# Optimization experiments

Measured on AMD Instinct MI355X. Metric: run time of the kernel, lower is better.

The kernel has to match this reference:

```python
import jax, jax.numpy as jnp
import numpy as np
from jax import lax

SIGMA, RHO, BETA = 10.0, 28.0, 8.0 / 3.0
DT = 0.01
LEN_VAR = 3
BATCH = 262144
T_STEPS = 64


def lorenz(x, t):
    # x: [3, B] -> dx/dt: [3, B]  (autonomous; t unused, kept for signature fidelity)
    xx, yy, zz = x[0], x[1], x[2]
    return jnp.stack([SIGMA * (yy - xx),
                      xx * (RHO - zz) - yy,
                      xx * yy - BETA * zz])


def tangent_propagator(x, dt):
    # Jfunc: returns I + dt * J(x), shape [3, 3, B]
    xx, yy, zz = x[0], x[1], x[2]
    o = jnp.ones_like(xx)
    z = jnp.zeros_like(xx)
    J = jnp.stack([
        jnp.stack([-SIGMA * o, SIGMA * o, z]),
        jnp.stack([RHO - zz, -o, -xx]),
        jnp.stack([yy, xx, -BETA * o]),
    ])  # [3,3,B]
    eye = jnp.eye(LEN_VAR, dtype=x.dtype)[:, :, None]
    return eye + dt * J


def ode4(x, t, dt):
    k1 = lorenz(x, t)
    k2 = lorenz(x + dt * 0.5 * k1, t + dt * 0.5)
    k3 = lorenz(x + dt * 0.5 * k2, t + dt * 0.5)
    # NOTE: faithful to original bug — k4 evaluated at x + dt*k2 (not k3)
    k4 = lorenz(x + dt * k2, t + dt)
    return x + dt * (k1 + 2.0 * k2 + 2.0 * k3 + k4) * (1.0 / 6.0)


def mgs_rows(M):
    # Modified Gram-Schmidt over rows of M: [lv, lv, B].
    # Matches in-place torch semantics: row kase is projected against the
    # already-orthogonalized (unnormalized) earlier rows.
    rows = [M[i] for i in range(LEN_VAR)]
    for kase in range(LEN_VAR):
        a = rows[kase]
        for i in range(kase):
            b = rows[i]
            coef = jnp.sum(b * a, axis=0) / jnp.sum(b * b, axis=0)  # [B]
            a = a - coef * b
        rows[kase] = a
    return jnp.stack(rows)  # [lv, lv, B]


def setup_inputs() -> dict:
    key = jax.random.key(0)
    x = jax.random.normal(key, (LEN_VAR, BATCH), dtype=jnp.float32)
    time_sequ = (jnp.arange(T_STEPS, dtype=jnp.float32) * DT)
    return {"x": x, "time_sequ": time_sequ}


def reference(x, time_sequ):
    dt = jnp.asarray(DT, dtype=x.dtype)
    B = x.shape[1]
    Q0 = jnp.broadcast_to(jnp.eye(LEN_VAR, dtype=x.dtype)[:, :, None],
                          (LEN_VAR, LEN_VAR, B))
    lya0 = jnp.zeros((LEN_VAR, B), dtype=x.dtype)

    def step(carry, t):
        xs, Q, lya = carry
        xs = ode4(xs, t, dt)
        J = tangent_propagator(xs, dt)           # [3,3,B]
        Q = jnp.einsum('ikb,kjb->ijb', J, Q)      # Jaco @ eye, per trajectory
        Q = mgs_rows(Q)
        norm = jnp.sqrt(jnp.sum(Q * Q, axis=1))   # [3,B] row norms
        Q = Q / norm[:, None, :]
        lya = (lya * t + jnp.log(norm)) / (t + dt)
        return (xs, Q, lya), None

    (xf, Qf, lya), _ = lax.scan(step, (x, Q0, lya0), time_sequ)
    return lya, xf
```

## Files before the change

kernel.cpp:

```cpp
#include <hip/hip_runtime.h>

#define SIGMA 10.0f
#define RHO   28.0f
#define DT    0.01f
static constexpr float BETA = (float)(8.0 / 3.0);
#define HALF_LN2 0.34657359028f

typedef float v2 __attribute__((ext_vector_type(2)));

__device__ __forceinline__ v2 vsplat(float s) { v2 r; r.x = s; r.y = s; return r; }
__device__ __forceinline__ v2 vfma(v2 a, v2 b, v2 c) {
    return __builtin_elementwise_fma(a, b, c);
}
__device__ __forceinline__ v2 sfma(float s, v2 a, v2 c) {
    return __builtin_elementwise_fma(vsplat(s), a, c);
}
__device__ __forceinline__ v2 vdot3(v2 a0, v2 a1, v2 a2, v2 b0, v2 b1, v2 b2) {
    return vfma(a2, b2, vfma(a1, b1, a0 * b0));
}
__device__ __forceinline__ v2 vrsq(v2 a) {
    v2 r;
    r.x = __builtin_amdgcn_rsqf(a.x);
    r.y = __builtin_amdgcn_rsqf(a.y);
    return r;
}

__device__ __forceinline__ void lorenz_v(v2 x, v2 y, v2 z,
                                         v2& dx, v2& dy, v2& dz) {
    dx = vsplat(SIGMA) * (y - x);
    dy = x * (vsplat(RHO) - z) - y;
    dz = x * y - vsplat(BETA) * z;
}

__global__ __launch_bounds__(256, 2)
void lya_spec_kernel(const float* __restrict__ xin,
                     const float* __restrict__ ts,
                     float* __restrict__ out,
                     int B, int T) {
    const int i = blockIdx.x * blockDim.x + threadIdx.x;
    if (2 * i >= B) return;

    v2 x = ((const v2*)(xin))[i];
    v2 y = ((const v2*)(xin + B))[i];
    v2 z = ((const v2*)(xin + 2 * B))[i];

    v2 q00 = vsplat(1.f), q01 = vsplat(0.f), q02 = vsplat(0.f);
    v2 q10 = vsplat(0.f), q11 = vsplat(1.f), q12 = vsplat(0.f);
    v2 q20 = vsplat(0.f), q21 = vsplat(0.f), q22 = vsplat(1.f);

    v2 pr0 = vsplat(1.f), pr1 = vsplat(1.f), pr2 = vsplat(1.f);

    for (int it = 0; it < T; ++it) {
        v2 k1x, k1y, k1z, k2x, k2y, k2z, k3x, k3y, k3z, k4x, k4y, k4z;
        lorenz_v(x, y, z, k1x, k1y, k1z);
        const float h = DT * 0.5f;
        lorenz_v(sfma(h, k1x, x), sfma(h, k1y, y), sfma(h, k1z, z), k2x, k2y, k2z);
        lorenz_v(sfma(h, k2x, x), sfma(h, k2y, y), sfma(h, k2z, z), k3x, k3y, k3z);
        lorenz_v(sfma(DT, k2x, x), sfma(DT, k2y, y), sfma(DT, k2z, z), k4x, k4y, k4z);
        const float c6 = DT * (float)(1.0 / 6.0);
        x = sfma(c6, (k1x + k4x) + vsplat(2.f) * (k2x + k3x), x);
        y = sfma(c6, (k1y + k4y) + vsplat(2.f) * (k2y + k3y), y);
        z = sfma(c6, (k1z + k4z) + vsplat(2.f) * (k2z + k3z), z);

        const float j00 = 1.0f - DT * SIGMA;
        const float j01 = DT * SIGMA;
        const float j11 = 1.0f - DT;
        const float j22 = 1.0f - DT * BETA;
        v2 j10 = vsplat(DT) * (vsplat(RHO) - z);
        v2 j12 = vsplat(-DT) * x;
        v2 j20 = vsplat(DT) * y;
        v2 j21 = vsplat(DT) * x;

        v2 n00 = sfma(j01, q10, vsplat(j00) * q00);
        v2 n01 = sfma(j01, q11, vsplat(j00) * q01);
        v2 n02 = sfma(j01, q12, vsplat(j00) * q02);
        v2 n10 = vfma(j12, q20, sfma(j11, q10, j10 * q00));
        v2 n11 = vfma(j12, q21, sfma(j11, q11, j10 * q01));
        v2 n12 = vfma(j12, q22, sfma(j11, q12, j10 * q02));
        v2 n20 = sfma(j22, q20, vfma(j21, q10, j20 * q00));
        v2 n21 = sfma(j22, q21, vfma(j21, q11, j20 * q01));
        v2 n22 = sfma(j22, q22, vfma(j21, q12, j20 * q02));

        v2 d00 = vdot3(n00, n01, n02, n00, n01, n02);
        v2 rn0 = vrsq(d00);
        v2 rd00 = rn0 * rn0;

        v2 d01 = vdot3(n00, n01, n02, n10, n11, n12);
        v2 c01 = d01 * rd00;
        v2 r10 = n10 - c01 * n00;
        v2 r11 = n11 - c01 * n01;
        v2 r12 = n12 - c01 * n02;

        v2 d02 = vdot3(n00, n01, n02, n20, n21, n22);
        v2 c02 = d02 * rd00;
        v2 a0 = n20 - c02 * n00;
        v2 a1 = n21 - c02 * n01;
        v2 a2 = n22 - c02 * n02;

        v2 d11 = vdot3(r10, r11, r12, r10, r11, r12);
        v2 rn1 = vrsq(d11);
        v2 d1a = vdot3(r10, r11, r12, a0, a1, a2);
        v2 c12 = d1a * (rn1 * rn1);
        v2 r20 = a0 - c12 * r10;
        v2 r21 = a1 - c12 * r11;
        v2 r22 = a2 - c12 * r12;

        v2 d22 = vdot3(r20, r21, r22, r20, r21, r22);
        v2 rn2 = vrsq(d22);

        pr0 = pr0 * d00;
        pr1 = pr1 * d11;
        pr2 = pr2 * d22;

        q00 = n00 * rn0; q01 = n01 * rn0; q02 = n02 * rn0;
        q10 = r10 * rn1; q11 = r11 * rn1; q12 = r12 * rn1;
        q20 = r20 * rn2; q21 = r21 * rn2; q22 = r22 * rn2;
    }

    const float denom = ts[T - 1] + DT;
    const float rden = __builtin_amdgcn_rcpf(denom) * HALF_LN2;
    v2 l0, l1, l2;
    l0.x = __builtin_amdgcn_logf(pr0.x) * rden;
    l0.y = __builtin_amdgcn_logf(pr0.y) * rden;
    l1.x = __builtin_amdgcn_logf(pr1.x) * rden;
    l1.y = __builtin_amdgcn_logf(pr1.y) * rden;
    l2.x = __builtin_amdgcn_logf(pr2.x) * rden;
    l2.y = __builtin_amdgcn_logf(pr2.y) * rden;

    ((v2*)(out))[i]          = l0;
    ((v2*)(out + B))[i]      = l1;
    ((v2*)(out + 2 * B))[i]  = l2;
    ((v2*)(out + 3 * B))[i]  = x;
    ((v2*)(out + 4 * B))[i]  = y;
    ((v2*)(out + 5 * B))[i]  = z;
}

extern "C" void kernel_launch(void* const* d_in, const int* in_sizes, int n_in,
                              void* d_out, int out_size, void* d_ws, size_t ws_size,
                              hipStream_t stream) {
    const float* xin = (const float*)d_in[0];
    const float* ts  = (const float*)d_in[1];
    float* out = (float*)d_out;

    const int B = in_sizes[0] / 3;
    const int T = in_sizes[1];

    const int block = 256;
    const int pairs = B / 2;
    const int grid = (pairs + block - 1) / block;
    lya_spec_kernel<<<grid, block, 0, stream>>>(xin, ts, out, B, T);
}
```

Baseline: 87.87 us.

## Software-pipeline RK4 one step ahead and compute Gram-Schmidt via Gram matrix

The RK4 state update for the next step is hoisted so it runs interleaved with the tangent-space QR of the current step, giving the scheduler two independent dependency chains to overlap. Modified Gram-Schmidt is recomputed from the 3x3 Gram matrix of the propagated rows, so all dot products are independent and the rsq chain is shorter. The cost is one extra RK4 evaluation per thread and altered floating-point rounding from the Gram-matrix formulation, which can lose accuracy when rows become nearly dependent.

```diff
diff --git a/kernel.cpp b/kernel.cpp
--- a/kernel.cpp
+++ b/kernel.cpp
@@ -32,6 +32,19 @@
     dz = x * y - vsplat(BETA) * z;
 }
 
+__device__ __forceinline__ void rk4(v2& x, v2& y, v2& z) {
+    v2 k1x, k1y, k1z, k2x, k2y, k2z, k3x, k3y, k3z, k4x, k4y, k4z;
+    lorenz_v(x, y, z, k1x, k1y, k1z);
+    const float h = DT * 0.5f;
+    lorenz_v(sfma(h, k1x, x), sfma(h, k1y, y), sfma(h, k1z, z), k2x, k2y, k2z);
+    lorenz_v(sfma(h, k2x, x), sfma(h, k2y, y), sfma(h, k2z, z), k3x, k3y, k3z);
+    lorenz_v(sfma(DT, k2x, x), sfma(DT, k2y, y), sfma(DT, k2z, z), k4x, k4y, k4z);
+    const float c6 = DT * (float)(1.0 / 6.0);
+    x = sfma(c6, (k1x + k4x) + vsplat(2.f) * (k2x + k3x), x);
+    y = sfma(c6, (k1y + k4y) + vsplat(2.f) * (k2y + k3y), y);
+    z = sfma(c6, (k1z + k4z) + vsplat(2.f) * (k2z + k3z), z);
+}
+
 __global__ __launch_bounds__(256, 2)
 void lya_spec_kernel(const float* __restrict__ xin,
                      const float* __restrict__ ts,
@@ -40,9 +53,9 @@
     const int i = blockIdx.x * blockDim.x + threadIdx.x;
     if (2 * i >= B) return;
 
-    v2 x = ((const v2*)(xin))[i];
-    v2 y = ((const v2*)(xin + B))[i];
-    v2 z = ((const v2*)(xin + 2 * B))[i];
+    v2 xn = ((const v2*)(xin))[i];
+    v2 yn = ((const v2*)(xin + B))[i];
+    v2 zn = ((const v2*)(xin + 2 * B))[i];
 
     v2 q00 = vsplat(1.f), q01 = vsplat(0.f), q02 = vsplat(0.f);
     v2 q10 = vsplat(0.f), q11 = vsplat(1.f), q12 = vsplat(0.f);
@@ -50,26 +63,18 @@
 
     v2 pr0 = vsplat(1.f), pr1 = vsplat(1.f), pr2 = vsplat(1.f);
 
+    rk4(xn, yn, zn);
+    v2 xo = xn, yo = yn, zo = zn;
+
     for (int it = 0; it < T; ++it) {
-        v2 k1x, k1y, k1z, k2x, k2y, k2z, k3x, k3y, k3z, k4x, k4y, k4z;
-        lorenz_v(x, y, z, k1x, k1y, k1z);
-        const float h = DT * 0.5f;
-        lorenz_v(sfma(h, k1x, x), sfma(h, k1y, y), sfma(h, k1z, z), k2x, k2y, k2z);
-        lorenz_v(sfma(h, k2x, x), sfma(h, k2y, y), sfma(h, k2z, z), k3x, k3y, k3z);
-        lorenz_v(sfma(DT, k2x, x), sfma(DT, k2y, y), sfma(DT, k2z, z), k4x, k4y, k4z);
-        const float c6 = DT * (float)(1.0 / 6.0);
-        x = sfma(c6, (k1x + k4x) + vsplat(2.f) * (k2x + k3x), x);
-        y = sfma(c6, (k1y + k4y) + vsplat(2.f) * (k2y + k3y), y);
-        z = sfma(c6, (k1z + k4z) + vsplat(2.f) * (k2z + k3z), z);
-
         const float j00 = 1.0f - DT * SIGMA;
         const float j01 = DT * SIGMA;
         const float j11 = 1.0f - DT;
         const float j22 = 1.0f - DT * BETA;
-        v2 j10 = vsplat(DT) * (vsplat(RHO) - z);
-        v2 j12 = vsplat(-DT) * x;
-        v2 j20 = vsplat(DT) * y;
-        v2 j21 = vsplat(DT) * x;
+        v2 j10 = vsplat(DT) * (vsplat(RHO) - zn);
+        v2 j12 = vsplat(-DT) * xn;
+        v2 j20 = vsplat(DT) * yn;
+        v2 j21 = vsplat(DT) * xn;
 
         v2 n00 = sfma(j01, q10, vsplat(j00) * q00);
         v2 n01 = sfma(j01, q11, vsplat(j00) * q01);
@@ -81,36 +86,38 @@
         v2 n21 = sfma(j22, q21, vfma(j21, q11, j20 * q01));
         v2 n22 = sfma(j22, q22, vfma(j21, q12, j20 * q02));
 
-        v2 d00 = vdot3(n00, n01, n02, n00, n01, n02);
-        v2 rn0 = vrsq(d00);
+        xo = xn; yo = yn; zo = zn;
+        rk4(xn, yn, zn);
+
+        v2 g00 = vdot3(n00, n01, n02, n00, n01, n02);
+        v2 g01 = vdot3(n00, n01, n02, n10, n11, n12);
+        v2 g02 = vdot3(n00, n01, n02, n20, n21, n22);
+        v2 g11 = vdot3(n10, n11, n12, n10, n11, n12);
+        v2 g12 = vdot3(n10, n11, n12, n20, n21, n22);
+        v2 g22 = vdot3(n20, n21, n22, n20, n21, n22);
+
+        v2 rn0 = vrsq(g00);
         v2 rd00 = rn0 * rn0;
+        v2 c01 = g01 * rd00;
+        v2 c02 = g02 * rd00;
 
-        v2 d01 = vdot3(n00, n01, n02, n10, n11, n12);
-        v2 c01 = d01 * rd00;
+        v2 e11 = g11 - c01 * g01;
+        v2 m12 = g12 - c01 * g02;
+        v2 rn1 = vrsq(e11);
+        v2 c12 = m12 * (rn1 * rn1);
+        v2 e22 = (g22 - c02 * g02) - c12 * m12;
+        v2 rn2 = vrsq(e22);
+
         v2 r10 = n10 - c01 * n00;
         v2 r11 = n11 - c01 * n01;
         v2 r12 = n12 - c01 * n02;
+        v2 r20 = (n20 - c02 * n00) - c12 * r10;
+        v2 r21 = (n21 - c02 * n01) - c12 * r11;
+        v2 r22 = (n22 - c02 * n02) - c12 * r12;
 
-        v2 d02 = vdot3(n00, n01, n02, n20, n21, n22);
-        v2 c02 = d02 * rd00;
-        v2 a0 = n20 - c02 * n00;
-        v2 a1 = n21 - c02 * n01;
-        v2 a2 = n22 - c02 * n02;
-
-        v2 d11 = vdot3(r10, r11, r12, r10, r11, r12);
-        v2 rn1 = vrsq(d11);
-        v2 d1a = vdot3(r10, r11, r12, a0, a1, a2);
-        v2 c12 = d1a * (rn1 * rn1);
-        v2 r20 = a0 - c12 * r10;
-        v2 r21 = a1 - c12 * r11;
-        v2 r22 = a2 - c12 * r12;
-
-        v2 d22 = vdot3(r20, r21, r22, r20, r21, r22);
-        v2 rn2 = vrsq(d22);
-
-        pr0 = pr0 * d00;
-        pr1 = pr1 * d11;
-        pr2 = pr2 * d22;
+        pr0 = pr0 * g00;
+        pr1 = pr1 * e11;
+        pr2 = pr2 * e22;
 
         q00 = n00 * rn0; q01 = n01 * rn0; q02 = n02 * rn0;
         q10 = r10 * rn1; q11 = r11 * rn1; q12 = r12 * rn1;
@@ -130,9 +137,9 @@
     ((v2*)(out))[i]          = l0;
     ((v2*)(out + B))[i]      = l1;
     ((v2*)(out + 2 * B))[i]  = l2;
-    ((v2*)(out + 3 * B))[i]  = x;
-    ((v2*)(out + 4 * B))[i]  = y;
-    ((v2*)(out + 5 * B))[i]  = z;
+    ((v2*)(out + 3 * B))[i]  = xo;
+    ((v2*)(out + 4 * B))[i]  = yo;
+    ((v2*)(out + 5 * B))[i]  = zo;
 }
 
 extern "C" void kernel_launch(void* const* d_in, const int* in_sizes, int n_in,
```

After: 88.99 us. About the same (+1.3%).
